# Optimization experiments

Measured on AMD Instinct MI355X. Metric: run time of the kernel, lower is better.

The kernel has to match this reference:

```python
import jax, jax.numpy as jnp
import numpy as np

# Config matching init_kwargs: lat_size=512, fin=64, fout=64, fhidden=128,
# dim=2, kernel_size=1, stride=1, padding=0, groups=1, lat_factor=1.
B, FIN, FOUT, FHID, H, W = 16, 64, 64, 128, 128, 128
LAT = 512
LS = 512            # self.lat_size (lat_size > 3 so unchanged) * lat_factor
HID1 = 1024         # LinearResidualBlock default hidden = fin + fout
HID2 = 1024         # second LRB hidden = self.lat_size * lat_factor * 2
SIZES = [FHID*FIN, FHID*FHID, FOUT*FHID, FOUT*FIN, FHID, FHID, FOUT, FOUT]
KTOT = int(np.sum(SIZES))  # 37248
OFFS = np.cumsum([0] + SIZES)


def setup_inputs() -> dict:
    key = jax.random.key(0)
    ks = jax.random.split(key, 10)
    def w(k, shape):
        return (jax.random.normal(k, shape, jnp.float32) / np.sqrt(shape[0])).astype(jnp.float32)
    return {
        "x": jax.random.normal(ks[0], (B, FIN, H, W), jnp.float32),
        "lat": jax.random.normal(ks[1], (B, LAT), jnpp := jnp.float32) if False else jax.random.normal(ks[1], (B, LAT), jnp.float32),
        # dyna_k = Linear(LAT, LS) -> LRB(LS, LS) -> LRB(LS, KTOT, hidden=HID2)
        "dk_w": w(ks[2], (LAT, LS)), "dk_b": jnp.zeros((LS,), jnp.float32),
        "l1_w1": w(ks[3], (LS, HID1)), "l1_b1": jnp.zeros((HID1,), jnp.float32),
        "l1_w2": w(ks[4], (HID1, LS)), "l1_b2": jnp.zeros((LS,), jnp.float32),
        "l2_w1": w(ks[5], (LS, HID2)), "l2_b1": jnp.zeros((HID2,), jnp.float32),
        "l2_w2": w(ks[6], (HID2, KTOT)), "l2_b2": jnp.zeros((KTOT,), jnp.float32),
        "l2_ws": w(ks[7], (LS, KTOT)),  # shortcut linear (fin != fout)
    }


def _lrb(h, w1, b1, w2, b2, ws=None):
    # LinearResidualBlock: shortcut(h) + Linear(ReLU(Linear(h)))
    sc = h if ws is None else h @ ws
    return sc + jax.nn.relu(h @ w1 + b1) @ w2 + b2


def _hyper(lat, dk_w, dk_b, l1_w1, l1_b1, l1_w2, l1_b2, l2_w1, l2_b1, l2_w2, l2_b2, l2_ws):
    h = lat @ dk_w + dk_b
    h = _lrb(h, l1_w1, l1_b1, l1_w2, l1_b2)          # fin == fout -> identity shortcut
    return _lrb(h, l2_w1, l2_b1, l2_w2, l2_b2, l2_ws)


def _dyna_block(x, ksv):
    # Split hypernet output into per-sample 1x1 conv kernels and biases.
    k_in = ksv[:, OFFS[0]:OFFS[1]].reshape(B, FHID, FIN)
    k_mid = ksv[:, OFFS[1]:OFFS[2]].reshape(B, FHID, FHID)
    k_out = ksv[:, OFFS[2]:OFFS[3]].reshape(B, FOUT, FHID)
    k_sh = ksv[:, OFFS[3]:OFFS[4]].reshape(B, FOUT, FIN)
    b_in = ksv[:, OFFS[4]:OFFS[5]][:, :, None, None]
    b_mid = ksv[:, OFFS[5]:OFFS[6]][:, :, None, None]
    b_out = ksv[:, OFFS[6]:OFFS[7]][:, :, None, None]
    b_sh = ksv[:, OFFS[7]:OFFS[8]][:, :, None, None]
    # groups = batch trick == per-sample 1x1 conv == batched channel GEMM
    xs = jnp.einsum('boi,bihw->bohw', k_sh, x) + b_sh
    hh = jax.nn.relu(jnp.einsum('boi,bihw->bohw', k_in, x) + b_in)
    hh = jax.nn.relu(jnp.einsum('boi,bihw->bohw', k_mid, hh) + b_mid)
    return jnp.einsum('boi,bihw->bohw', k_out, hh) + b_out + xs


def reference(x, lat, dk_w, dk_b, l1_w1, l1_b1, l1_w2, l1_b2, l2_w1, l2_b1, l2_w2, l2_b2, l2_ws):
    ksv = _hyper(lat, dk_w, dk_b, l1_w1, l1_b1, l1_w2, l1_b2, l2_w1, l2_b1, l2_w2, l2_b2, l2_ws)
    return _dyna_block(x, ksv)  # [B, FOUT, H, W]
```

## Files before the change

### kernel.cpp

```cpp
#include <hip/hip_runtime.h>

#define N_KSV 37248
#define N_KW  36864

typedef float f32x4 __attribute__((ext_vector_type(4)));
typedef short short8 __attribute__((ext_vector_type(8)));
typedef short short4v __attribute__((ext_vector_type(4)));
typedef __bf16 bf16x8 __attribute__((ext_vector_type(8)));

__device__ inline short f2bs(float f) {
  unsigned u = __builtin_bit_cast(unsigned, f);
  u += 0x7fffu + ((u >> 16) & 1u);
  return (short)(u >> 16);
}

__device__ inline f32x4 mfma16(short8 a, short8 b, f32x4 c) {
  return __builtin_amdgcn_mfma_f32_16x16x32_bf16(
      __builtin_bit_cast(bf16x8, a), __builtin_bit_cast(bf16x8, b), c, 0, 0, 0);
}

__global__ void k_h0(const float* __restrict__ lat, const float* __restrict__ w,
                     const float* __restrict__ bias, float* __restrict__ h0) {
  int j = blockIdx.x * 256 + threadIdx.x;
  int b = blockIdx.y;
  const float* lp = lat + b * 512;
  float acc = bias[j];
#pragma unroll 16
  for (int k = 0; k < 512; ++k) acc = fmaf(lp[k], w[k * 512 + j], acc);
  h0[b * 512 + j] = acc;
}

__global__ void k_t1(const float* __restrict__ h0, const float* __restrict__ w,
                     const float* __restrict__ bias, float* __restrict__ t1) {
  int j = blockIdx.x * 256 + threadIdx.x;
  int b = blockIdx.y;
  const float* hp = h0 + b * 512;
  float acc = bias[j];
#pragma unroll 16
  for (int k = 0; k < 512; ++k) acc = fmaf(hp[k], w[k * 1024 + j], acc);
  t1[b * 1024 + j] = fmaxf(acc, 0.f);
}

__global__ void k_h(const float* __restrict__ h0, const float* __restrict__ t1,
                    const float* __restrict__ w, const float* __restrict__ bias,
                    float* __restrict__ h, short* __restrict__ hxT) {
  int j = blockIdx.x * 256 + threadIdx.x;
  int b = blockIdx.y;
  const float* tp = t1 + b * 1024;
  float acc = bias[j];
#pragma unroll 16
  for (int k = 0; k < 1024; ++k) acc = fmaf(tp[k], w[k * 512 + j], acc);
  float v = acc + h0[b * 512 + j];
  h[b * 512 + j] = v;
  hxT[b * 1536 + j] = f2bs(v);
}

__global__ void k_t2(const float* __restrict__ h, const float* __restrict__ w,
                     const float* __restrict__ bias, short* __restrict__ hxT) {
  int j = blockIdx.x * 256 + threadIdx.x;
  int b = blockIdx.y;
  const float* hp = h + b * 512;
  float acc = bias[j];
#pragma unroll 16
  for (int k = 0; k < 512; ++k) acc = fmaf(hp[k], w[k * 1024 + j], acc);
  hxT[b * 1536 + 512 + j] = f2bs(fmaxf(acc, 0.f));
}

#define LOADB(dst, ktv) { \
    const float* bp_ = ((ktv) < 16) ? (wsp + (size_t)((ktv) * 32) * N_KSV) \
                                    : (w2p + (size_t)((ktv) * 32 - 512) * N_KSV); \
    dst[0] = *reinterpret_cast<const f32x4*>(bp_); \
    dst[1] = *reinterpret_cast<const f32x4*>(bp_ + (size_t)1 * N_KSV); \
    dst[2] = *reinterpret_cast<const f32x4*>(bp_ + (size_t)2 * N_KSV); \
    dst[3] = *reinterpret_cast<const f32x4*>(bp_ + (size_t)3 * N_KSV); \
    dst[4] = *reinterpret_cast<const f32x4*>(bp_ + (size_t)4 * N_KSV); \
    dst[5] = *reinterpret_cast<const f32x4*>(bp_ + (size_t)5 * N_KSV); \
    dst[6] = *reinterpret_cast<const f32x4*>(bp_ + (size_t)6 * N_KSV); \
    dst[7] = *reinterpret_cast<const f32x4*>(bp_ + (size_t)7 * N_KSV); }

#define LOADA(dst, ktv) \
    dst = *reinterpret_cast<const short8*>(apb + (ktv) * 32);

#define COMPUTE(bsrc, asrc) { \
    _Pragma("unroll") \
    for (int t = 0; t < 4; ++t) { \
      short8 bf_; \
      bf_[0] = f2bs(bsrc[0][t]); bf_[1] = f2bs(bsrc[1][t]); \
      bf_[2] = f2bs(bsrc[2][t]); bf_[3] = f2bs(bsrc[3][t]); \
      bf_[4] = f2bs(bsrc[4][t]); bf_[5] = f2bs(bsrc[5][t]); \
      bf_[6] = f2bs(bsrc[6][t]); bf_[7] = f2bs(bsrc[7][t]); \
      acc[t] = mfma16(asrc, bf_, acc[t]); \
    } }

__global__ __launch_bounds__(256, 4) void k5_mfma(
    const float* __restrict__ wsm, const float* __restrict__ w2,
    const short* __restrict__ hxT, const float* __restrict__ b2,
    float* __restrict__ ksv, short* __restrict__ kwb) {
  __shared__ f32x4 red[3][64][4];
  const int tid = threadIdx.x;
  const int wv = tid >> 6;
  const int lane = tid & 63;
  const int col0 = blockIdx.x * 64;
  const int l15 = lane & 15;
  const int lg = lane >> 4;

  const float* wsp = wsm + (size_t)(lg * 8) * N_KSV + col0 + l15 * 4;
  const float* w2p = w2 + (size_t)(lg * 8) * N_KSV + col0 + l15 * 4;
  const short* apb = hxT + l15 * 1536 + lg * 8;

  f32x4 acc[4];
#pragma unroll
  for (int t = 0; t < 4; ++t) acc[t] = (f32x4){0.f, 0.f, 0.f, 0.f};

  const int kt0 = wv * 12;
  f32x4 bA[8], bB[8];
  short8 aA, aB;
  LOADB(bA, kt0);
  LOADA(aA, kt0);

#pragma unroll
  for (int s = 0; s < 12; ++s) {
    if (s + 1 < 12) {
      if ((s & 1) == 0) {
        LOADB(bB, kt0 + s + 1);
        LOADA(aB, kt0 + s + 1);
      } else {
        LOADB(bA, kt0 + s + 1);
        LOADA(aA, kt0 + s + 1);
      }
    }
    if ((s & 1) == 0) COMPUTE(bA, aA) else COMPUTE(bB, aB)
  }

  if (wv > 0) {
#pragma unroll
    for (int t = 0; t < 4; ++t) red[wv - 1][lane][t] = acc[t];
  }
  __syncthreads();
  if (wv != 0) return;

#pragma unroll
  for (int t = 0; t < 4; ++t) {
    acc[t] += red[0][lane][t];
    acc[t] += red[1][lane][t];
    acc[t] += red[2][lane][t];
  }

  const int m0 = lg * 4;
#pragma unroll
  for (int t = 0; t < 4; ++t) {
    const int col = col0 + l15 * 4 + t;
    const float bias = b2[col];
#pragma unroll
    for (int r = 0; r < 4; ++r) {
      float s = acc[t][r] + bias;
      ksv[(size_t)(m0 + r) * N_KSV + col] = s;
      if (col < N_KW)
        kwb[(size_t)(m0 + r) * N_KW + col] = f2bs(s);
    }
  }
}

__device__ inline int xT_idx(int p, int c) {
  return p * 64 + ((((c >> 3) ^ (p & 7)) << 3) | (c & 7));
}
__device__ inline int h_idx(int p, int c) {
  return p * 128 + ((((c >> 3) ^ (p & 7)) << 3) | (c & 7));
}

__global__ __launch_bounds__(256) void k_dyna(const float* __restrict__ x,
                                              const short* __restrict__ kwb,
                                              const float* __restrict__ ksv,
                                              float* __restrict__ out) {
  __shared__ __align__(16) short lds[20480];
  short* xT = lds;
  short* h1 = lds + 4096;
  short* h2 = lds + 12288;
  float* sout = reinterpret_cast<float*>(h1);

  const int tid = threadIdx.x;
  const int lane = tid & 63;
  const int w = tid >> 6;
  const int l15 = lane & 15;
  const int lg = lane >> 4;

  const int b = blockIdx.x >> 8;
  const int pos0 = (blockIdx.x & 255) << 6;

  const float* xb = x + ((size_t)b << 20) + pos0;
  const short* kw = kwb + b * N_KW;
  const float* bias = ksv + (size_t)b * N_KSV + N_KW;

#pragma unroll
  for (int i = 0; i < 8; ++i) {
    int p = lane;
    int cp = i * 4 + w;
    int c = cp * 2;
    float v0 = __builtin_nontemporal_load(xb + (size_t)c * 16384 + p);
    float v1 = __builtin_nontemporal_load(xb + (size_t)(c + 1) * 16384 + p);
    int idx = xT_idx(p, c);
    int pk = (int)(unsigned short)f2bs(v0) | ((int)f2bs(v1) << 16);
    *reinterpret_cast<int*>(&xT[idx]) = pk;
  }
  __syncthreads();

  short8 a1[2][2];
#pragma unroll
  for (int mt = 0; mt < 2; ++mt)
#pragma unroll
    for (int kf = 0; kf < 2; ++kf)
      a1[mt][kf] = *reinterpret_cast<const short8*>(
          kw + (w * 32 + mt * 16 + l15) * 64 + kf * 32 + lg * 8);

  f32x4 zero = {0.f, 0.f, 0.f, 0.f};
  f32x4 acc1[2][4];
#pragma unroll
  for (int mt = 0; mt < 2; ++mt)
#pragma unroll
    for (int nt = 0; nt < 4; ++nt) acc1[mt][nt] = zero;

#pragma unroll
  for (int nt = 0; nt < 4; ++nt) {
    int p = nt * 16 + l15;
    short8 b0 = *reinterpret_cast<const short8*>(&xT[xT_idx(p, lg * 8)]);
    short8 b1 = *reinterpret_cast<const short8*>(&xT[xT_idx(p, 32 + lg * 8)]);
#pragma unroll
    for (int mt = 0; mt < 2; ++mt) {
      acc1[mt][nt] = mfma16(a1[mt][0], b0, acc1[mt][nt]);
      acc1[mt][nt] = mfma16(a1[mt][1], b1, acc1[mt][nt]);
    }
  }
#pragma unroll
  for (int mt = 0; mt < 2; ++mt) {
    int ch0 = w * 32 + mt * 16 + lg * 4;
    f32x4 bv = *reinterpret_cast<const f32x4*>(bias + ch0);
#pragma unroll
    for (int nt = 0; nt < 4; ++nt) {
      int p = nt * 16 + l15;
      short4v hv;
#pragma unroll
      for (int jj = 0; jj < 4; ++jj)
        hv[jj] = f2bs(fmaxf(acc1[mt][nt][jj] + bv[jj], 0.f));
      *reinterpret_cast<short4v*>(&h1[h_idx(p, ch0)]) = hv;
    }
  }
  __syncthreads();

  short8 a2[2][4];
#pragma unroll
  for (int mt = 0; mt < 2; ++mt)
#pragma unroll
    for (int kf = 0; kf < 4; ++kf)
      a2[mt][kf] = *reinterpret_cast<const short8*>(
          kw + 8192 + (w * 32 + mt * 16 + l15) * 128 + kf * 32 + lg * 8);

  f32x4 acc2[2][4];
#pragma unroll
  for (int mt = 0; mt < 2; ++mt)
#pragma unroll
    for (int nt = 0; nt < 4; ++nt) acc2[mt][nt] = zero;

#pragma unroll
  for (int nt = 0; nt < 4; ++nt) {
    int p = nt * 16 + l15;
    short8 bb[4];
#pragma unroll
    for (int kf = 0; kf < 4; ++kf)
      bb[kf] = *reinterpret_cast<const short8*>(&h1[h_idx(p, kf * 32 + lg * 8)]);
#pragma unroll
    for (int mt = 0; mt < 2; ++mt)
#pragma unroll
      for (int kf = 0; kf < 4; ++kf)
        acc2[mt][nt] = mfma16(a2[mt][kf], bb[kf], acc2[mt][nt]);
  }
#pragma unroll
  for (int mt = 0; mt < 2; ++mt) {
    int ch0 = w * 32 + mt * 16 + lg * 4;
    f32x4 bv = *reinterpret_cast<const f32x4*>(bias + 128 + ch0);
#pragma unroll
    for (int nt = 0; nt < 4; ++nt) {
      int p = nt * 16 + l15;
      short4v hv;
#pragma unroll
      for (int jj = 0; jj < 4; ++jj)
        hv[jj] = f2bs(fmaxf(acc2[mt][nt][jj] + bv[jj], 0.f));
      *reinterpret_cast<short4v*>(&h2[h_idx(p, ch0)]) = hv;
    }
  }
  __syncthreads();

  short8 a3[4], ash[2];
#pragma unroll
  for (int kf = 0; kf < 4; ++kf)
    a3[kf] = *reinterpret_cast<const short8*>(
        kw + 24576 + (w * 16 + l15) * 128 + kf * 32 + lg * 8);
#pragma unroll
  for (int kf = 0; kf < 2; ++kf)
    ash[kf] = *reinterpret_cast<const short8*>(
        kw + 32768 + (w * 16 + l15) * 64 + kf * 32 + lg * 8);

  int ch0 = w * 16 + lg * 4;
  f32x4 bo = *reinterpret_cast<const f32x4*>(bias + 256 + ch0);
  f32x4 bs = *reinterpret_cast<const f32x4*>(bias + 320 + ch0);

#pragma unroll
  for (int nt = 0; nt < 4; ++nt) {
    int p = nt * 16 + l15;
    f32x4 acc = zero;
#pragma unroll
    for (int kf = 0; kf < 4; ++kf) {
      short8 bb = *reinterpret_cast<const short8*>(&h2[h_idx(p, kf * 32 + lg * 8)]);
      acc = mfma16(a3[kf], bb, acc);
    }
#pragma unroll
    for (int kf = 0; kf < 2; ++kf) {
      short8 bb = *reinterpret_cast<const short8*>(&xT[xT_idx(p, kf * 32 + lg * 8)]);
      acc = mfma16(ash[kf], bb, acc);
    }
#pragma unroll
    for (int jj = 0; jj < 4; ++jj) {
      int ch = ch0 + jj;
      sout[(ch << 6) | (p ^ ((ch & 7) << 3))] = acc[jj] + bo[jj] + bs[jj];
    }
  }
  __syncthreads();

  float* outp = out + (((size_t)b * 64) << 14) + pos0;
#pragma unroll
  for (int i = 0; i < 4; ++i) {
    int flat = i * 1024 + tid * 4;
    int ch = flat >> 6;
    int p = flat & 63;
    f32x4 v = *reinterpret_cast<const f32x4*>(
        &sout[(ch << 6) | (p ^ ((ch & 7) << 3))]);
    __builtin_nontemporal_store(v,
        reinterpret_cast<f32x4*>(outp + ((size_t)ch << 14) + p));
  }
}

extern "C" void kernel_launch(void* const* d_in, const int* in_sizes, int n_in,
                              void* d_out, int out_size, void* d_ws, size_t ws_size,
                              hipStream_t stream) {
  const float* x    = (const float*)d_in[0];
  const float* lat  = (const float*)d_in[1];
  const float* dk_w = (const float*)d_in[2];
  const float* dk_b = (const float*)d_in[3];
  const float* l1w1 = (const float*)d_in[4];
  const float* l1b1 = (const float*)d_in[5];
  const float* l1w2 = (const float*)d_in[6];
  const float* l1b2 = (const float*)d_in[7];
  const float* l2w1 = (const float*)d_in[8];
  const float* l2b1 = (const float*)d_in[9];
  const float* l2w2 = (const float*)d_in[10];
  const float* l2b2 = (const float*)d_in[11];
  const float* l2ws = (const float*)d_in[12];
  float* out = (float*)d_out;
  float* wsf = (float*)d_ws;

  float* h0  = wsf;
  float* t1  = wsf + 8192;
  float* h   = wsf + 24576;
  float* ksv = wsf + 32768;
  short* hxT = (short*)(wsf + 628736);
  short* kwb = hxT + 24576;

  k_h0<<<dim3(2, 16), 256, 0, stream>>>(lat, dk_w, dk_b, h0);
  k_t1<<<dim3(4, 16), 256, 0, stream>>>(h0, l1w1, l1b1, t1);
  k_h <<<dim3(2, 16), 256, 0, stream>>>(h0, t1, l1w2, l1b2, h, hxT);
  k_t2<<<dim3(4, 16), 256, 0, stream>>>(h, l2w1, l2b1, hxT);
  k5_mfma<<<dim3(N_KSV / 64), 256, 0, stream>>>(l2ws, l2w2, hxT, l2b2, ksv, kwb);
  k_dyna<<<dim3(4096), 256, 0, stream>>>(x, kwb, ksv, out);
}
```

Baseline: 187.9 us.

## Precompute bf16 transposed x inside hypernet GEMM launch to overlap work

The fp32-to-bf16 conversion and transpose of x move out of k_dyna into extra blocks of the k5 GEMM kernel. Those blocks write a pre-swizzled bf16 layout to workspace, so the x conversion runs alongside the weight-bound hypernet GEMM. k_dyna then reads its MFMA B operands directly from global memory, with no LDS staging and one fewer barrier. The cost is an extra round trip of the bf16 x through memory, about 32MB written and read back, plus uncoalesced-ish global short8 loads in k_dyna.

```diff
diff --git a/kernel.cpp b/kernel.cpp
--- a/kernel.cpp
+++ b/kernel.cpp
@@ -2,6 +2,8 @@
 
 #define N_KSV 37248
 #define N_KW  36864
+#define K5_BLOCKS 582
+#define XP_BLOCKS 1024
 
 typedef float f32x4 __attribute__((ext_vector_type(4)));
 typedef short short8 __attribute__((ext_vector_type(8)));
@@ -12,6 +14,10 @@
   unsigned u = __builtin_bit_cast(unsigned, f);
   u += 0x7fffu + ((u >> 16) & 1u);
   return (short)(u >> 16);
+}
+
+__device__ inline f32x4 ntl4(const float* p) {
+  return __builtin_nontemporal_load(reinterpret_cast<const f32x4*>(p));
 }
 
 __device__ inline f32x4 mfma16(short8 a, short8 b, f32x4 c) {
@@ -92,90 +98,130 @@
       acc[t] = mfma16(asrc, bf_, acc[t]); \
     } }
 
-__global__ __launch_bounds__(256, 4) void k5_mfma(
+__global__ __launch_bounds__(256, 4) void k5_fused(
     const float* __restrict__ wsm, const float* __restrict__ w2,
     const short* __restrict__ hxT, const float* __restrict__ b2,
-    float* __restrict__ ksv, short* __restrict__ kwb) {
-  __shared__ f32x4 red[3][64][4];
+    const float* __restrict__ x,
+    float* __restrict__ ksv, short* __restrict__ kwb,
+    short* __restrict__ xTw) {
+  __shared__ __align__(16) char smem[32768];
   const int tid = threadIdx.x;
-  const int wv = tid >> 6;
-  const int lane = tid & 63;
-  const int col0 = blockIdx.x * 64;
-  const int l15 = lane & 15;
-  const int lg = lane >> 4;
-
-  const float* wsp = wsm + (size_t)(lg * 8) * N_KSV + col0 + l15 * 4;
-  const float* w2p = w2 + (size_t)(lg * 8) * N_KSV + col0 + l15 * 4;
-  const short* apb = hxT + l15 * 1536 + lg * 8;
-
-  f32x4 acc[4];
-#pragma unroll
-  for (int t = 0; t < 4; ++t) acc[t] = (f32x4){0.f, 0.f, 0.f, 0.f};
-
-  const int kt0 = wv * 12;
-  f32x4 bA[8], bB[8];
-  short8 aA, aB;
-  LOADB(bA, kt0);
-  LOADA(aA, kt0);
-
-#pragma unroll
-  for (int s = 0; s < 12; ++s) {
-    if (s + 1 < 12) {
-      if ((s & 1) == 0) {
-        LOADB(bB, kt0 + s + 1);
-        LOADA(aB, kt0 + s + 1);
-      } else {
-        LOADB(bA, kt0 + s + 1);
-        LOADA(aA, kt0 + s + 1);
+
+  if (blockIdx.x < K5_BLOCKS) {
+    f32x4 (*red)[64][4] = reinterpret_cast<f32x4 (*)[64][4]>(smem);
+    const int wv = tid >> 6;
+    const int lane = tid & 63;
+    const int col0 = blockIdx.x * 64;
+    const int l15 = lane & 15;
+    const int lg = lane >> 4;
+
+    const float* wsp = wsm + (size_t)(lg * 8) * N_KSV + col0 + l15 * 4;
+    const float* w2p = w2 + (size_t)(lg * 8) * N_KSV + col0 + l15 * 4;
+    const short* apb = hxT + l15 * 1536 + lg * 8;
+
+    f32x4 acc[4];
+#pragma unroll
+    for (int t = 0; t < 4; ++t) acc[t] = (f32x4){0.f, 0.f, 0.f, 0.f};
+
+    const int kt0 = wv * 12;
+    f32x4 bA[8], bB[8];
+    short8 aA, aB;
+    LOADB(bA, kt0);
+    LOADA(aA, kt0);
+
+#pragma unroll
+    for (int s = 0; s < 12; ++s) {
+      if (s + 1 < 12) {
+        if ((s & 1) == 0) {
+          LOADB(bB, kt0 + s + 1);
+          LOADA(aB, kt0 + s + 1);
+        } else {
+          LOADB(bA, kt0 + s + 1);
+          LOADA(aA, kt0 + s + 1);
+        }
       }
-    }
-    if ((s & 1) == 0) COMPUTE(bA, aA) else COMPUTE(bB, aB)
-  }
-
-  if (wv > 0) {
-#pragma unroll
-    for (int t = 0; t < 4; ++t) red[wv - 1][lane][t] = acc[t];
-  }
-  __syncthreads();
-  if (wv != 0) return;
-
-#pragma unroll
-  for (int t = 0; t < 4; ++t) {
-    acc[t] += red[0][lane][t];
-    acc[t] += red[1][lane][t];
-    acc[t] += red[2][lane][t];
-  }
-
-  const int m0 = lg * 4;
-#pragma unroll
-  for (int t = 0; t < 4; ++t) {
-    const int col = col0 + l15 * 4 + t;
-    const float bias = b2[col];
-#pragma unroll
-    for (int r = 0; r < 4; ++r) {
-      float s = acc[t][r] + bias;
-      ksv[(size_t)(m0 + r) * N_KSV + col] = s;
-      if (col < N_KW)
-        kwb[(size_t)(m0 + r) * N_KW + col] = f2bs(s);
-    }
-  }
-}
-
-__device__ inline int xT_idx(int p, int c) {
-  return p * 64 + ((((c >> 3) ^ (p & 7)) << 3) | (c & 7));
-}
+      if ((s & 1) == 0) COMPUTE(bA, aA) else COMPUTE(bB, aB)
+    }
+
+    if (wv > 0) {
+#pragma unroll
+      for (int t = 0; t < 4; ++t) red[wv - 1][lane][t] = acc[t];
+    }
+    __syncthreads();
+    if (wv != 0) return;
+
+#pragma unroll
+    for (int t = 0; t < 4; ++t) {
+      acc[t] += red[0][lane][t];
+      acc[t] += red[1][lane][t];
+      acc[t] += red[2][lane][t];
+    }
+
+    const int m0 = lg * 4;
+#pragma unroll
+    for (int t = 0; t < 4; ++t) {
+      const int col = col0 + l15 * 4 + t;
+      const float bias = b2[col];
+#pragma unroll
+      for (int r = 0; r < 4; ++r) {
+        float s = acc[t][r] + bias;
+        ksv[(size_t)(m0 + r) * N_KSV + col] = s;
+        if (col < N_KW)
+          kwb[(size_t)(m0 + r) * N_KW + col] = f2bs(s);
+      }
+    }
+  } else {
+    short* lsh = reinterpret_cast<short*>(smem);
+    const int bx = blockIdx.x - K5_BLOCKS;
+    const int b = bx >> 6;
+    const int s = bx & 63;
+    const int pos0 = s << 8;
+
+    const float* xb = x + ((size_t)b << 20);
+    const int cc = (tid >> 3) * 2;
+    const int pc = (tid & 7) * 32;
+    const float* r0 = xb + (size_t)cc * 16384 + pos0 + pc;
+    const float* r1 = r0 + 16384;
+
+    f32x4 v0[8], v1[8];
+#pragma unroll
+    for (int i = 0; i < 8; ++i) v0[i] = ntl4(r0 + i * 4);
+#pragma unroll
+    for (int i = 0; i < 8; ++i) v1[i] = ntl4(r1 + i * 4);
+
+    const int cg = cc >> 3;
+    const int j = cc & 7;
+#pragma unroll
+    for (int p = 0; p < 32; ++p) {
+      int pk = (int)(unsigned short)f2bs(v0[p >> 2][p & 3]) |
+               ((int)f2bs(v1[p >> 2][p & 3]) << 16);
+      *reinterpret_cast<int*>(&lsh[cg * 2048 + (pc + p) * 8 + j]) = pk;
+    }
+    __syncthreads();
+
+    short* dst = xTw + (size_t)(b * 256 + s * 4) * 4096;
+#pragma unroll
+    for (int i = 0; i < 8; ++i) {
+      int q = i * 2048 + tid * 8;
+      int t_ = q >> 12, r_ = q & 4095;
+      int cg_ = r_ >> 9, rem = r_ & 511;
+      *reinterpret_cast<short8*>(dst + q) =
+          *reinterpret_cast<const short8*>(&lsh[cg_ * 2048 + t_ * 512 + rem]);
+    }
+  }
+}
+
 __device__ inline int h_idx(int p, int c) {
   return p * 128 + ((((c >> 3) ^ (p & 7)) << 3) | (c & 7));
 }
 
-__global__ __launch_bounds__(256) void k_dyna(const float* __restrict__ x,
+__global__ __launch_bounds__(256) void k_dyna(const short* __restrict__ xTw,
                                               const short* __restrict__ kwb,
                                               const float* __restrict__ ksv,
                                               float* __restrict__ out) {
-  __shared__ __align__(16) short lds[20480];
-  short* xT = lds;
-  short* h1 = lds + 4096;
-  short* h2 = lds + 12288;
+  __shared__ __align__(16) short lds[16384];
+  short* h1 = lds;
+  short* h2 = lds + 8192;
   float* sout = reinterpret_cast<float*>(h1);
 
   const int tid = threadIdx.x;
@@ -185,24 +231,12 @@
   const int lg = lane >> 4;
 
   const int b = blockIdx.x >> 8;
-  const int pos0 = (blockIdx.x & 255) << 6;
-
-  const float* xb = x + ((size_t)b << 20) + pos0;
+  const int tg = blockIdx.x & 255;
+  const int pos0 = tg << 6;
+
+  const short* xw = xTw + (size_t)(b * 256 + tg) * 4096;
   const short* kw = kwb + b * N_KW;
   const float* bias = ksv + (size_t)b * N_KSV + N_KW;
-
-#pragma unroll
-  for (int i = 0; i < 8; ++i) {
-    int p = lane;
-    int cp = i * 4 + w;
-    int c = cp * 2;
-    float v0 = __builtin_nontemporal_load(xb + (size_t)c * 16384 + p);
-    float v1 = __builtin_nontemporal_load(xb + (size_t)(c + 1) * 16384 + p);
-    int idx = xT_idx(p, c);
-    int pk = (int)(unsigned short)f2bs(v0) | ((int)f2bs(v1) << 16);
-    *reinterpret_cast<int*>(&xT[idx]) = pk;
-  }
-  __syncthreads();
 
   short8 a1[2][2];
 #pragma unroll
@@ -221,9 +255,10 @@
 
 #pragma unroll
   for (int nt = 0; nt < 4; ++nt) {
-    int p = nt * 16 + l15;
-    short8 b0 = *reinterpret_cast<const short8*>(&xT[xT_idx(p, lg * 8)]);
-    short8 b1 = *reinterpret_cast<const short8*>(&xT[xT_idx(p, 32 + lg * 8)]);
+    short8 b0 = *reinterpret_cast<const short8*>(
+        xw + lg * 512 + (nt * 16 + l15) * 8);
+    short8 b1 = *reinterpret_cast<const short8*>(
+        xw + (4 + lg) * 512 + (nt * 16 + l15) * 8);
 #pragma unroll
     for (int mt = 0; mt < 2; ++mt) {
       acc1[mt][nt] = mfma16(a1[mt][0], b0, acc1[mt][nt]);
@@ -314,7 +349,8 @@
     }
 #pragma unroll
     for (int kf = 0; kf < 2; ++kf) {
-      short8 bb = *reinterpret_cast<const short8*>(&xT[xT_idx(p, kf * 32 + lg * 8)]);
+      short8 bb = *reinterpret_cast<const short8*>(
+          xw + (kf * 4 + lg) * 512 + (nt * 16 + l15) * 8);
       acc = mfma16(ash[kf], bb, acc);
     }
 #pragma unroll
@@ -363,11 +399,13 @@
   float* ksv = wsf + 32768;
   short* hxT = (short*)(wsf + 628736);
   short* kwb = hxT + 24576;
+  short* xTw = kwb + (size_t)16 * N_KW;
 
   k_h0<<<dim3(2, 16), 256, 0, stream>>>(lat, dk_w, dk_b, h0);
   k_t1<<<dim3(4, 16), 256, 0, stream>>>(h0, l1w1, l1b1, t1);
   k_h <<<dim3(2, 16), 256, 0, stream>>>(h0, t1, l1w2, l1b2, h, hxT);
   k_t2<<<dim3(4, 16), 256, 0, stream>>>(h, l2w1, l2b1, hxT);
-  k5_mfma<<<dim3(N_KSV / 64), 256, 0, stream>>>(l2ws, l2w2, hxT, l2b2, ksv, kwb);
-  k_dyna<<<dim3(4096), 256, 0, stream>>>(x, kwb, ksv, out);
-}
+  k5_fused<<<dim3(K5_BLOCKS + XP_BLOCKS), 256, 0, stream>>>(
+      l2ws, l2w2, hxT, l2b2, x, ksv, kwb, xTw);
+  k_dyna<<<dim3(4096), 256, 0, stream>>>(xTw, kwb, ksv, out);
+}
```

New measurement: 237.7 us. 1.27x slower.

## Halve dyna tile to 32 pixels, restructure loops for lower registers and LDS

Applied to the files above, without the earlier changes.

The per-sample conv kernel now processes 32 spatial positions per block instead of 64, doubling the grid to 8192 blocks and halving LDS. The GEMM loops are restructured to handle one 16-channel tile at a time, so only one accumulator is live rather than big accumulator arrays, and launch bounds request 8 blocks per CU. The aim is higher occupancy to hide memory latency in this bandwidth-bound kernel. In exchange, each block reloads the full per-sample weights for half the pixels, which doubles weight-fetch traffic and per-block overhead.

```diff
diff --git a/kernel.cpp b/kernel.cpp
--- a/kernel.cpp
+++ b/kernel.cpp
@@ -168,14 +168,14 @@
   return p * 128 + ((((c >> 3) ^ (p & 7)) << 3) | (c & 7));
 }
 
-__global__ __launch_bounds__(256) void k_dyna(const float* __restrict__ x,
-                                              const short* __restrict__ kwb,
-                                              const float* __restrict__ ksv,
-                                              float* __restrict__ out) {
-  __shared__ __align__(16) short lds[20480];
+__global__ __launch_bounds__(256, 8) void k_dyna(const float* __restrict__ x,
+                                                 const short* __restrict__ kwb,
+                                                 const float* __restrict__ ksv,
+                                                 float* __restrict__ out) {
+  __shared__ __align__(16) short lds[10240];
   short* xT = lds;
-  short* h1 = lds + 4096;
-  short* h2 = lds + 12288;
+  short* h1 = lds + 2048;
+  short* h2 = lds + 6144;
   float* sout = reinterpret_cast<float*>(h1);
 
   const int tid = threadIdx.x;
@@ -184,155 +184,125 @@
   const int l15 = lane & 15;
   const int lg = lane >> 4;
 
-  const int b = blockIdx.x >> 8;
-  const int pos0 = (blockIdx.x & 255) << 6;
+  const int b = blockIdx.x >> 9;
+  const int tg = blockIdx.x & 511;
+  const int pos0 = tg << 5;
 
   const float* xb = x + ((size_t)b << 20) + pos0;
   const short* kw = kwb + b * N_KW;
   const float* bias = ksv + (size_t)b * N_KSV + N_KW;
 
 #pragma unroll
-  for (int i = 0; i < 8; ++i) {
-    int p = lane;
-    int cp = i * 4 + w;
+  for (int i = 0; i < 4; ++i) {
+    int cp = i * 8 + w * 2 + (lane >> 5);
+    int p = lane & 31;
     int c = cp * 2;
     float v0 = __builtin_nontemporal_load(xb + (size_t)c * 16384 + p);
     float v1 = __builtin_nontemporal_load(xb + (size_t)(c + 1) * 16384 + p);
-    int idx = xT_idx(p, c);
     int pk = (int)(unsigned short)f2bs(v0) | ((int)f2bs(v1) << 16);
-    *reinterpret_cast<int*>(&xT[idx]) = pk;
-  }
-  __syncthreads();
-
-  short8 a1[2][2];
-#pragma unroll
-  for (int mt = 0; mt < 2; ++mt)
+    *reinterpret_cast<int*>(&xT[xT_idx(p, c)]) = pk;
+  }
+  __syncthreads();
+
+  f32x4 zero = {0.f, 0.f, 0.f, 0.f};
+
+#pragma unroll
+  for (int ctl = 0; ctl < 2; ++ctl) {
+    int ct = w * 2 + ctl;
+    short8 a10 = *reinterpret_cast<const short8*>(kw + (ct * 16 + l15) * 64 + lg * 8);
+    short8 a11 = *reinterpret_cast<const short8*>(kw + (ct * 16 + l15) * 64 + 32 + lg * 8);
+    int ch0 = ct * 16 + lg * 4;
+    f32x4 bv = *reinterpret_cast<const f32x4*>(bias + ch0);
+#pragma unroll
+    for (int nt = 0; nt < 2; ++nt) {
+      int p = nt * 16 + l15;
+      short8 b0 = *reinterpret_cast<const short8*>(&xT[xT_idx(p, lg * 8)]);
+      short8 b1 = *reinterpret_cast<const short8*>(&xT[xT_idx(p, 32 + lg * 8)]);
+      f32x4 acc = mfma16(a10, b0, zero);
+      acc = mfma16(a11, b1, acc);
+      short4v hv;
+#pragma unroll
+      for (int jj = 0; jj < 4; ++jj)
+        hv[jj] = f2bs(fmaxf(acc[jj] + bv[jj], 0.f));
+      *reinterpret_cast<short4v*>(&h1[h_idx(p, ch0)]) = hv;
+    }
+  }
+  __syncthreads();
+
+#pragma unroll
+  for (int ctl = 0; ctl < 2; ++ctl) {
+    int ct = w * 2 + ctl;
+    short8 a2[4];
+#pragma unroll
+    for (int kf = 0; kf < 4; ++kf)
+      a2[kf] = *reinterpret_cast<const short8*>(
+          kw + 8192 + (ct * 16 + l15) * 128 + kf * 32 + lg * 8);
+    int ch0 = ct * 16 + lg * 4;
+    f32x4 bv = *reinterpret_cast<const f32x4*>(bias + 128 + ch0);
+#pragma unroll
+    for (int nt = 0; nt < 2; ++nt) {
+      int p = nt * 16 + l15;
+      f32x4 acc = zero;
+#pragma unroll
+      for (int kf = 0; kf < 4; ++kf) {
+        short8 bb = *reinterpret_cast<const short8*>(&h1[h_idx(p, kf * 32 + lg * 8)]);
+        acc = mfma16(a2[kf], bb, acc);
+      }
+      short4v hv;
+#pragma unroll
+      for (int jj = 0; jj < 4; ++jj)
+        hv[jj] = f2bs(fmaxf(acc[jj] + bv[jj], 0.f));
+      *reinterpret_cast<short4v*>(&h2[h_idx(p, ch0)]) = hv;
+    }
+  }
+  __syncthreads();
+
+  {
+    short8 a3[4], ash[2];
+#pragma unroll
+    for (int kf = 0; kf < 4; ++kf)
+      a3[kf] = *reinterpret_cast<const short8*>(
+          kw + 24576 + (w * 16 + l15) * 128 + kf * 32 + lg * 8);
 #pragma unroll
     for (int kf = 0; kf < 2; ++kf)
-      a1[mt][kf] = *reinterpret_cast<const short8*>(
-          kw + (w * 32 + mt * 16 + l15) * 64 + kf * 32 + lg * 8);
-
-  f32x4 zero = {0.f, 0.f, 0.f, 0.f};
-  f32x4 acc1[2][4];
-#pragma unroll
-  for (int mt = 0; mt < 2; ++mt)
-#pragma unroll
-    for (int nt = 0; nt < 4; ++nt) acc1[mt][nt] = zero;
-
-#pragma unroll
-  for (int nt = 0; nt < 4; ++nt) {
-    int p = nt * 16 + l15;
-    short8 b0 = *reinterpret_cast<const short8*>(&xT[xT_idx(p, lg * 8)]);
-    short8 b1 = *reinterpret_cast<const short8*>(&xT[xT_idx(p, 32 + lg * 8)]);
-#pragma unroll
-    for (int mt = 0; mt < 2; ++mt) {
-      acc1[mt][nt] = mfma16(a1[mt][0], b0, acc1[mt][nt]);
-      acc1[mt][nt] = mfma16(a1[mt][1], b1, acc1[mt][nt]);
-    }
-  }
-#pragma unroll
-  for (int mt = 0; mt < 2; ++mt) {
-    int ch0 = w * 32 + mt * 16 + lg * 4;
-    f32x4 bv = *reinterpret_cast<const f32x4*>(bias + ch0);
-#pragma unroll
-    for (int nt = 0; nt < 4; ++nt) {
+      ash[kf] = *reinterpret_cast<const short8*>(
+          kw + 32768 + (w * 16 + l15) * 64 + kf * 32 + lg * 8);
+
+    int ch0 = w * 16 + lg * 4;
+    f32x4 bo = *reinterpret_cast<const f32x4*>(bias + 256 + ch0);
+    f32x4 bs = *reinterpret_cast<const f32x4*>(bias + 320 + ch0);
+
+#pragma unroll
+    for (int nt = 0; nt < 2; ++nt) {
       int p = nt * 16 + l15;
-      short4v hv;
-#pragma unroll
-      for (int jj = 0; jj < 4; ++jj)
-        hv[jj] = f2bs(fmaxf(acc1[mt][nt][jj] + bv[jj], 0.f));
-      *reinterpret_cast<short4v*>(&h1[h_idx(p, ch0)]) = hv;
-    }
-  }
-  __syncthreads();
-
-  short8 a2[2][4];
-#pragma unroll
-  for (int mt = 0; mt < 2; ++mt)
-#pragma unroll
-    for (int kf = 0; kf < 4; ++kf)
-      a2[mt][kf] = *reinterpret_cast<const short8*>(
-          kw + 8192 + (w * 32 + mt * 16 + l15) * 128 + kf * 32 + lg * 8);
-
-  f32x4 acc2[2][4];
-#pragma unroll
-  for (int mt = 0; mt < 2; ++mt)
-#pragma unroll
-    for (int nt = 0; nt < 4; ++nt) acc2[mt][nt] = zero;
-
-#pragma unroll
-  for (int nt = 0; nt < 4; ++nt) {
-    int p = nt * 16 + l15;
-    short8 bb[4];
-#pragma unroll
-    for (int kf = 0; kf < 4; ++kf)
-      bb[kf] = *reinterpret_cast<const short8*>(&h1[h_idx(p, kf * 32 + lg * 8)]);
-#pragma unroll
-    for (int mt = 0; mt < 2; ++mt)
-#pragma unroll
-      for (int kf = 0; kf < 4; ++kf)
-        acc2[mt][nt] = mfma16(a2[mt][kf], bb[kf], acc2[mt][nt]);
-  }
-#pragma unroll
-  for (int mt = 0; mt < 2; ++mt) {
-    int ch0 = w * 32 + mt * 16 + lg * 4;
-    f32x4 bv = *reinterpret_cast<const f32x4*>(bias + 128 + ch0);
-#pragma unroll
-    for (int nt = 0; nt < 4; ++nt) {
-      int p = nt * 16 + l15;
-      short4v hv;
-#pragma unroll
-      for (int jj = 0; jj < 4; ++jj)
-        hv[jj] = f2bs(fmaxf(acc2[mt][nt][jj] + bv[jj], 0.f));
-      *reinterpret_cast<short4v*>(&h2[h_idx(p, ch0)]) = hv;
-    }
-  }
-  __syncthreads();
-
-  short8 a3[4], ash[2];
-#pragma unroll
-  for (int kf = 0; kf < 4; ++kf)
-    a3[kf] = *reinterpret_cast<const short8*>(
-        kw + 24576 + (w * 16 + l15) * 128 + kf * 32 + lg * 8);
-#pragma unroll
-  for (int kf = 0; kf < 2; ++kf)
-    ash[kf] = *reinterpret_cast<const short8*>(
-        kw + 32768 + (w * 16 + l15) * 64 + kf * 32 + lg * 8);
-
-  int ch0 = w * 16 + lg * 4;
-  f32x4 bo = *reinterpret_cast<const f32x4*>(bias + 256 + ch0);
-  f32x4 bs = *reinterpret_cast<const f32x4*>(bias + 320 + ch0);
-
-#pragma unroll
-  for (int nt = 0; nt < 4; ++nt) {
-    int p = nt * 16 + l15;
-    f32x4 acc = zero;
-#pragma unroll
-    for (int kf = 0; kf < 4; ++kf) {
-      short8 bb = *reinterpret_cast<const short8*>(&h2[h_idx(p, kf * 32 + lg * 8)]);
-      acc = mfma16(a3[kf], bb, acc);
-    }
-#pragma unroll
-    for (int kf = 0; kf < 2; ++kf) {
-      short8 bb = *reinterpret_cast<const short8*>(&xT[xT_idx(p, kf * 32 + lg * 8)]);
-      acc = mfma16(ash[kf], bb, acc);
-    }
-#pragma unroll
-    for (int jj = 0; jj < 4; ++jj) {
-      int ch = ch0 + jj;
-      sout[(ch << 6) | (p ^ ((ch & 7) << 3))] = acc[jj] + bo[jj] + bs[jj];
+      f32x4 acc = zero;
+#pragma unroll
+      for (int kf = 0; kf < 4; ++kf) {
+        short8 bb = *reinterpret_cast<const short8*>(&h2[h_idx(p, kf * 32 + lg * 8)]);
+        acc = mfma16(a3[kf], bb, acc);
+      }
+#pragma unroll
+      for (int kf = 0; kf < 2; ++kf) {
+        short8 bb = *reinterpret_cast<const short8*>(&xT[xT_idx(p, kf * 32 + lg * 8)]);
+        acc = mfma16(ash[kf], bb, acc);
+      }
+#pragma unroll
+      for (int jj = 0; jj < 4; ++jj) {
+        int ch = ch0 + jj;
+        sout[(ch << 5) | (p ^ ((ch & 7) << 2))] = acc[jj] + bo[jj] + bs[jj];
+      }
     }
   }
   __syncthreads();
 
   float* outp = out + (((size_t)b * 64) << 14) + pos0;
 #pragma unroll
-  for (int i = 0; i < 4; ++i) {
+  for (int i = 0; i < 2; ++i) {
     int flat = i * 1024 + tid * 4;
-    int ch = flat >> 6;
-    int p = flat & 63;
+    int ch = flat >> 5;
+    int p = flat & 31;
     f32x4 v = *reinterpret_cast<const f32x4*>(
-        &sout[(ch << 6) | (p ^ ((ch & 7) << 3))]);
+        &sout[(ch << 5) | (p ^ ((ch & 7) << 2))]);
     __builtin_nontemporal_store(v,
         reinterpret_cast<f32x4*>(outp + ((size_t)ch << 14) + p));
   }
@@ -369,5 +339,5 @@
   k_h <<<dim3(2, 16), 256, 0, stream>>>(h0, t1, l1w2, l1b2, h, hxT);
   k_t2<<<dim3(4, 16), 256, 0, stream>>>(h, l2w1, l2b1, hxT);
   k5_mfma<<<dim3(N_KSV / 64), 256, 0, stream>>>(l2ws, l2w2, hxT, l2b2, ksv, kwb);
-  k_dyna<<<dim3(4096), 256, 0, stream>>>(x, kwb, ksv, out);
-}
+  k_dyna<<<dim3(8192), 256, 0, stream>>>(x, kwb, ksv, out);
+}
```

Measured after the change: 213.7 us. 13.7% more time.
